# Optimization experiments

Measured on AMD Instinct MI355X. Metric: run time of the kernel, lower is better.

Reference implementation:

```python
import jax, jax.numpy as jnp
import numpy as np

LN_EPS = 1e-5

def sin_emb(coords, dim):
    # coords [..., 3] -> [..., dim]; dim split evenly over 3 axes, sin/cos halves
    per_axis = dim // 3
    half = per_axis // 2
    freqs = jnp.exp(-jnp.log(10000.0) * jnp.arange(half, dtype=coords.dtype) / max(half - 1, 1))
    ang = coords[..., None] * freqs  # [..., 3, half]
    emb = jnp.concatenate([jnp.sin(ang), jnp.cos(ang)], axis=-1)  # [..., 3, per_axis]
    return emb.reshape(coords.shape[:-1] + (dim,))

def layernorm(x, g, b):
    mu = jnp.mean(x, axis=-1, keepdims=True)
    var = jnp.mean((x - mu) ** 2, axis=-1, keepdims=True)
    return (x - mu) * jax.lax.rsqrt(var + LN_EPS) * g + b

def point_mlp(x, w, b, g, be, act):
    h = layernorm(x @ w + b, g, be)
    return jax.nn.gelu(h, approximate=False) if act else h

def query_ball_point(radius, nsample, xyz):
    # xyz [B,N,3] -> idx [B,N,nsample] (pad with first in-ball index, PointNet++ style)
    N = xyz.shape[1]
    sq = jnp.sum((xyz[:, :, None, :] - xyz[:, None, :, :]) ** 2, axis=-1)  # [B,N,N]
    idx0 = jnp.where(sq > radius * radius, N, jnp.arange(N)[None, None, :])
    idx = jnp.sort(idx0, axis=-1)[:, :, :nsample]
    return jnp.where(idx == N, idx[:, :, :1], idx)

def index_points(points, idx):
    # points [B,N,C], idx [B,S,K] -> [B,S,K,C]
    return jax.vmap(lambda p, i: p[i])(points, idx)

def setup_inputs() -> dict:
    key = jax.random.key(0)
    ks = jax.random.split(key, 20)
    B, N, C_stem, C_tok = 4, 4096, 64, 256
    C_in = C_stem + 3 + 24 + 96  # 187
    w = lambda k, i, o: jax.random.normal(k, (i, o), jnp.float32) * 0.02
    inp = {
        'xyz': jax.random.uniform(ks[0], (B, N, 3), jnp.float32),
        'point_feature': jax.random.normal(ks[1], (B, N, C_stem), jnp.float32),
        # scene_point_mlp
        'w1': w(ks[2], C_in, C_tok), 'b1': jnp.zeros((C_tok,)), 'g1': jnp.ones((C_tok,)), 'be1': jnp.zeros((C_tok,)),
        'w2': w(ks[3], C_tok, C_tok), 'b2': jnp.zeros((C_tok,)), 'g2': jnp.ones((C_tok,)), 'be2': jnp.zeros((C_tok,)),
        # scene_projection
        'pw1': w(ks[4], C_tok, C_tok), 'pb1': jnp.zeros((C_tok,)), 'pg1': jnp.ones((C_tok,)), 'pbe1': jnp.zeros((C_tok,)),
        'pw2': w(ks[5], C_tok, C_tok), 'pb2': jnp.zeros((C_tok,)), 'pg2': jnp.ones((C_tok,)), 'pbe2': jnp.zeros((C_tok,)),
    }
    return inp

def reference(xyz, point_feature, w1, b1, g1, be1, w2, b2, g2, be2,
              pw1, pb1, pg1, pbe1, pw2, pb2, pg2, pbe2):
    radius, K = 0.16, 32
    idx = query_ball_point(radius, K, xyz)                     # [B,N,K]
    grouped_xyz = index_points(xyz, idx)                       # [B,N,K,3]
    grouped_feature = index_points(point_feature, idx)         # [B,N,K,Cs]
    relative_xyz = grouped_xyz - xyz[:, :, None, :]            # [B,N,K,3]
    relative_position = sin_emb(relative_xyz, 24)              # [B,N,K,24]
    absolute_position = sin_emb(xyz, 96)                       # [B,N,96]
    B, N = xyz.shape[0], xyz.shape[1]
    absolute_position = jnp.broadcast_to(absolute_position[:, :, None, :], (B, N, K, 96))
    grouped_input = jnp.concatenate(
        (grouped_feature, relative_xyz, relative_position, absolute_position), axis=-1)
    h = point_mlp(grouped_input, w1, b1, g1, be1, True)
    h = point_mlp(h, w2, b2, g2, be2, False)
    scene_point_feature = jnp.max(h, axis=2)                   # [B,N,C]
    pooled = jnp.max(scene_point_feature, axis=1, keepdims=True)  # [B,1,C]
    t = point_mlp(pooled, pw1, pb1, pg1, pbe1, True)
    global_scene_token = point_mlp(t, pw2, pb2, pg2, pbe2, False)
    return global_scene_token
```

## Files before the change

### kernel.cpp

```cpp
#include <hip/hip_runtime.h>
#include <hip/hip_bf16.h>
#include <math.h>


#define LN_EPS 1e-5f

typedef __attribute__((ext_vector_type(8))) short bf16x8;
typedef __attribute__((ext_vector_type(4))) float f32x4;
typedef __attribute__((ext_vector_type(2))) unsigned int u32x2;
typedef __attribute__((ext_vector_type(4))) unsigned int u32x4;

#if __has_builtin(__builtin_amdgcn_rcpf)
#define FRCP(x) __builtin_amdgcn_rcpf(x)
#else
#define FRCP(x) (1.0f / (x))
#endif

__device__ __forceinline__ unsigned short f2bf(float f) {
    unsigned int x = __float_as_uint(f);
    return (unsigned short)((x + 0x7FFFu + ((x >> 16) & 1u)) >> 16);
}
__device__ __forceinline__ unsigned int pack2(float a, float b) {
    union { __hip_bfloat162 h; unsigned int u; } cvt;
    cvt.h = __float22bfloat162_rn(make_float2(a, b));
    return cvt.u;
}
__device__ __forceinline__ unsigned int fenc(float f) {
    unsigned int u = __float_as_uint(f);
    return (u & 0x80000000u) ? ~u : (u | 0x80000000u);
}
__device__ __forceinline__ float fdec(unsigned int u) {
    return __uint_as_float((u & 0x80000000u) ? (u & 0x7FFFFFFFu) : ~u);
}
__device__ __forceinline__ float gelu_fast(float x) {
    float x2 = x * x;
    float u = x * fmaf(0.0356774081f, x2, 0.7978845608f);
    float e = exp2f(u * -2.8853900818f);
    float r = FRCP(e + 1.0f);
    return x * r;
}
template<int CTRL>
__device__ __forceinline__ float dppadd(float s) {
    int v = __builtin_amdgcn_update_dpp(0, __float_as_int(s), CTRL, 0xF, 0xF, true);
    return s + __int_as_float(v);
}
__device__ __forceinline__ float rowsum16(float x) {
    x = dppadd<0x128>(x);
    x = dppadd<0x124>(x);
    x = dppadd<0x122>(x);
    x = dppadd<0x121>(x);
    return x;
}

__global__ __launch_bounds__(256) void k_prep(
    const float* __restrict__ w1, const float* __restrict__ w2,
    unsigned short* __restrict__ w2T, unsigned short* __restrict__ w1aT,
    unsigned short* __restrict__ w1cT, unsigned short* __restrict__ w1bT,
    unsigned int* __restrict__ pooled, int* __restrict__ done)
{
    int t = threadIdx.x, blk = blockIdx.x;
    if (blk < 16) {
        __shared__ unsigned short tile[64][65];
        int tr = blk >> 2, tc = blk & 3;
        #pragma unroll
        for (int rr = 0; rr < 16; ++rr) {
            int kl = rr * 4 + (t >> 6), nl = t & 63;
            tile[kl][nl] = f2bf(w2[(size_t)(tr * 64 + kl) * 256 + tc * 64 + nl]);
        }
        __syncthreads();
        #pragma unroll
        for (int rr = 0; rr < 16; ++rr) {
            int nl = rr * 4 + (t >> 6), kp = t & 63;
            int kl = (kp & 3) * 16 + (kp >> 2);
            w2T[(size_t)(tc * 64 + nl) * 256 + tr * 64 + kp] = tile[kl][nl];
        }
    } else if (blk < 20) {
        __shared__ unsigned short tile[64][65];
        int tc = blk - 16;
        #pragma unroll
        for (int rr = 0; rr < 16; ++rr) {
            int kl = rr * 4 + (t >> 6), nl = t & 63;
            tile[kl][nl] = f2bf(w1[(size_t)kl * 256 + tc * 64 + nl]);
        }
        __syncthreads();
        #pragma unroll
        for (int rr = 0; rr < 16; ++rr) {
            int nl = rr * 4 + (t >> 6), kl = t & 63;
            w1aT[(size_t)(tc * 64 + nl) * 64 + kl] = tile[kl][nl];
        }
    } else if (blk < 28) {
        __shared__ unsigned short tile[64][65];
        int idx = blk - 20;
        int tr2 = idx >> 2, tc = idx & 3;
        #pragma unroll
        for (int rr = 0; rr < 16; ++rr) {
            int kl = rr * 4 + (t >> 6), nl = t & 63;
            int k = tr2 * 64 + kl;
            float v = 0.f;
            if (k < 96) v = w1[(size_t)(91 + k) * 256 + tc * 64 + nl];
            tile[kl][nl] = f2bf(v);
        }
        __syncthreads();
        #pragma unroll
        for (int rr = 0; rr < 16; ++rr) {
            int nl = rr * 4 + (t >> 6), kl = t & 63;
            int k = tr2 * 64 + kl;
            if (k < 96)
                w1cT[(size_t)(tc * 64 + nl) * 96 + k] = tile[kl][nl];
        }
    } else if (blk == 28) {
        int n = t;
        #pragma unroll
        for (int k = 0; k < 32; ++k) {
            unsigned short v = 0;
            if (k < 27) v = f2bf(w1[(size_t)(64 + k) * 256 + n]);
            w1bT[(size_t)n * 32 + k] = v;
        }
    } else {
        unsigned int idv = fenc(-1e19f);
        for (int q = t; q < 1024; q += 256) pooled[q] = idv;
        if (t == 0) *done = 0;
    }
}

__global__ __launch_bounds__(256) void k_pre(
    const float* __restrict__ xyz, const float* __restrict__ pf,
    const unsigned short* __restrict__ w1aT, const unsigned short* __restrict__ w1cT,
    const float* __restrict__ b1,
    float* __restrict__ U_p, float* __restrict__ V_p)
{
    __shared__ __align__(16) unsigned short ptile[64 * 72];
    __shared__ __align__(16) unsigned short etile[64 * 104];
    int tid = threadIdx.x, wv = tid >> 6, lane = tid & 63;
    int lo16 = lane & 15, quad = lane >> 4;
    int rows0 = blockIdx.x * 64;

    {
        int r = tid >> 2, seg = tid & 3;
        const f32x4* src = (const f32x4*)(pf + (size_t)(rows0 + r) * 64 + seg * 16);
        f32x4 v0 = src[0], v1 = src[1], v2 = src[2], v3 = src[3];
        u32x4 o0, o1;
        o0.x = pack2(v0.x, v0.y); o0.y = pack2(v0.z, v0.w);
        o0.z = pack2(v1.x, v1.y); o0.w = pack2(v1.z, v1.w);
        o1.x = pack2(v2.x, v2.y); o1.y = pack2(v2.z, v2.w);
        o1.z = pack2(v3.x, v3.y); o1.w = pack2(v3.z, v3.w);
        u32x4* dst = (u32x4*)&ptile[r * 72 + seg * 16];
        dst[0] = o0; dst[1] = o1;
    }
    {
        int r = tid & 63, grp = tid >> 6;
        float c0 = xyz[(size_t)(rows0 + r) * 3];
        float c1 = xyz[(size_t)(rows0 + r) * 3 + 1];
        float c2 = xyz[(size_t)(rows0 + r) * 3 + 2];
        #pragma unroll
        for (int q = 0; q < 12; ++q) {
            int pr = grp * 12 + q;
            float vals[2];
            #pragma unroll
            for (int qq = 0; qq < 2; ++qq) {
                int cc = pr * 2 + qq;
                int a = cc >> 5, wI = cc & 31;
                int jf = (wI < 16) ? wI : (wI - 16);
                float coord = (a == 0) ? c0 : ((a == 1) ? c1 : c2);
                float fr = __expf(-0.61402269146507894f * (float)jf);
                float ang = coord * fr;
                vals[qq] = (wI < 16) ? __sinf(ang) : __cosf(ang);
            }
            *(unsigned int*)&etile[r * 104 + 2 * pr] = pack2(vals[0], vals[1]);
        }
    }
    __syncthreads();

    f32x4 acc[4][4];
    #pragma unroll
    for (int mt = 0; mt < 4; ++mt)
        #pragma unroll
        for (int nt = 0; nt < 4; ++nt) acc[mt][nt] = (f32x4){0.f, 0.f, 0.f, 0.f};
    #pragma unroll
    for (int ks = 0; ks < 2; ++ks) {
        bf16x8 bfr[4];
        #pragma unroll
        for (int nt = 0; nt < 4; ++nt) {
            int n = wv * 64 + nt * 16 + lo16;
            bfr[nt] = *(const bf16x8*)&w1aT[(size_t)n * 64 + ks * 32 + quad * 8];
        }
        #pragma unroll
        for (int mt = 0; mt < 4; ++mt) {
            bf16x8 afr = *(const bf16x8*)&ptile[(mt * 16 + lo16) * 72 + ks * 32 + quad * 8];
            #pragma unroll
            for (int nt = 0; nt < 4; ++nt)
                acc[mt][nt] = __builtin_amdgcn_mfma_f32_16x16x32_bf16(
                    afr, bfr[nt], acc[mt][nt], 0, 0, 0);
        }
    }
    #pragma unroll
    for (int mt = 0; mt < 4; ++mt)
        #pragma unroll
        for (int reg = 0; reg < 4; ++reg) {
            f32x4 o = {acc[mt][0][reg], acc[mt][1][reg], acc[mt][2][reg], acc[mt][3][reg]};
            *(f32x4*)&U_p[(size_t)(rows0 + mt * 16 + quad * 4 + reg) * 256 + wv * 64 + lo16 * 4] = o;
        }

    {
        float b1f[4];
        #pragma unroll
        for (int nt = 0; nt < 4; ++nt) b1f[nt] = b1[wv * 64 + nt * 16 + lo16];
        #pragma unroll
        for (int mt = 0; mt < 4; ++mt)
            #pragma unroll
            for (int nt = 0; nt < 4; ++nt)
                #pragma unroll
                for (int reg = 0; reg < 4; ++reg) acc[mt][nt][reg] = b1f[nt];
    }
    #pragma unroll
    for (int ks = 0; ks < 3; ++ks) {
        bf16x8 bfr[4];
        #pragma unroll
        for (int nt = 0; nt < 4; ++nt) {
            int n = wv * 64 + nt * 16 + lo16;
            bfr[nt] = *(const bf16x8*)&w1cT[(size_t)n * 96 + ks * 32 + quad * 8];
        }
        #pragma unroll
        for (int mt = 0; mt < 4; ++mt) {
            bf16x8 afr = *(const bf16x8*)&etile[(mt * 16 + lo16) * 104 + ks * 32 + quad * 8];
            #pragma unroll
            for (int nt = 0; nt < 4; ++nt)
                acc[mt][nt] = __builtin_amdgcn_mfma_f32_16x16x32_bf16(
                    afr, bfr[nt], acc[mt][nt], 0, 0, 0);
        }
    }
    #pragma unroll
    for (int mt = 0; mt < 4; ++mt)
        #pragma unroll
        for (int reg = 0; reg < 4; ++reg) {
            f32x4 o = {acc[mt][0][reg], acc[mt][1][reg], acc[mt][2][reg], acc[mt][3][reg]};
            *(f32x4*)&V_p[(size_t)(rows0 + mt * 16 + quad * 4 + reg) * 256 + wv * 64 + lo16 * 4] = o;
        }
}

__global__ __launch_bounds__(512, 4) void k_main(
    const float* __restrict__ xyz,
    const unsigned short* __restrict__ w1bT, const unsigned short* __restrict__ w2T,
    const float* __restrict__ U_p, const float* __restrict__ V_p,
    const float* __restrict__ g1, const float* __restrict__ be1,
    const float* __restrict__ b2, const float* __restrict__ g2,
    const float* __restrict__ be2,
    unsigned int* __restrict__ pooled, int* __restrict__ done,
    const float* __restrict__ pw1, const float* __restrict__ pb1,
    const float* __restrict__ pg1, const float* __restrict__ pbe1,
    const float* __restrict__ pw2, const float* __restrict__ pb2,
    const float* __restrict__ pg2, const float* __restrict__ pbe2,
    float* __restrict__ out)
{
    __shared__ __align__(16) unsigned short smem[128 * 264];
    __shared__ unsigned long long bmask[4][64];
    __shared__ int   idxs[128];
    __shared__ float ctr[4][3];
    __shared__ float reds[128][4][2];
    __shared__ float musig[128][2];
    __shared__ int   lastf;
    unsigned short* rels = smem;
    unsigned short* h1s  = smem;

    const int N = 4096;
    int tid = threadIdx.x, wv = tid >> 6, lane = tid & 63;
    int lo16 = lane & 15, quad = lane >> 4;
    int wvM = wv >> 2, wvN = wv & 3;
    int b = blockIdx.x & 3;
    int i0 = (blockIdx.x >> 2) * 4;
    size_t base = (size_t)b * N;
    const float* xb = xyz + base * 3;

    bf16x8 bfrR[4];
    #pragma unroll
    for (int nt = 0; nt < 4; ++nt) {
        int n = wvN * 64 + nt * 16 + lo16;
        bfrR[nt] = *(const bf16x8*)&w1bT[(size_t)n * 32 + quad * 8];
    }

    if (tid < 12) { int p = tid / 3, a = tid - 3 * p; ctr[p][a] = xb[(i0 + p) * 3 + a]; }
    const double r2d = 0.16 * 0.16;
    float T = (float)r2d;
    if ((double)T > r2d) T = __uint_as_float(__float_as_uint(T) - 1u);
    {
        f32x4 cA = *(const f32x4*)(xb + (size_t)i0 * 3);
        f32x4 cB = *(const f32x4*)(xb + (size_t)i0 * 3 + 4);
        f32x4 cC = *(const f32x4*)(xb + (size_t)i0 * 3 + 8);
        float cx0 = cA.x, cy0 = cA.y, cz0 = cA.z;
        float cx1 = cA.w, cy1 = cB.x, cz1 = cB.y;
        float cx2 = cB.z, cy2 = cB.w, cz2 = cC.x;
        float cx3 = cC.y, cy3 = cC.z, cz3 = cC.w;
        #pragma unroll 2
        for (int i = 0; i < 8; ++i) {
            int chunk = wv * 8 + i;
            int j = chunk * 64 + lane;
            const float* pp = xb + (size_t)j * 3;
            float px = pp[0], py = pp[1], pz = pp[2];
            float dx0 = __fsub_rn(px, cx0), dy0 = __fsub_rn(py, cy0), dz0 = __fsub_rn(pz, cz0);
            float sq0 = __fadd_rn(__fadd_rn(__fmul_rn(dx0, dx0), __fmul_rn(dy0, dy0)),
                                  __fmul_rn(dz0, dz0));
            unsigned long long m0 = __ballot(sq0 <= T);
            float dx1 = __fsub_rn(px, cx1), dy1 = __fsub_rn(py, cy1), dz1 = __fsub_rn(pz, cz1);
            float sq1 = __fadd_rn(__fadd_rn(__fmul_rn(dx1, dx1), __fmul_rn(dy1, dy1)),
                                  __fmul_rn(dz1, dz1));
            unsigned long long m1 = __ballot(sq1 <= T);
            float dx2 = __fsub_rn(px, cx2), dy2 = __fsub_rn(py, cy2), dz2 = __fsub_rn(pz, cz2);
            float sq2 = __fadd_rn(__fadd_rn(__fmul_rn(dx2, dx2), __fmul_rn(dy2, dy2)),
                                  __fmul_rn(dz2, dz2));
            unsigned long long m2 = __ballot(sq2 <= T);
            float dx3 = __fsub_rn(px, cx3), dy3 = __fsub_rn(py, cy3), dz3 = __fsub_rn(pz, cz3);
            float sq3 = __fadd_rn(__fadd_rn(__fmul_rn(dx3, dx3), __fmul_rn(dy3, dy3)),
                                  __fmul_rn(dz3, dz3));
            unsigned long long m3 = __ballot(sq3 <= T);
            if (lane == 0) {
                bmask[0][chunk] = m0; bmask[1][chunk] = m1;
                bmask[2][chunk] = m2; bmask[3][chunk] = m3;
            }
        }
    }
    __syncthreads();
    if (wv < 4) {
        int p = wv;
        unsigned long long m = bmask[p][lane];
        int c = __popcll(m);
        int inc = c;
        #pragma unroll
        for (int d = 1; d <= 32; d <<= 1) {
            int v = __shfl_up(inc, d);
            if (lane >= d) inc += v;
        }
        int exc = inc - c;
        int total = __shfl(inc, 63);
        unsigned long long lm = __ballot(m != 0ull);
        int fl = __ffsll(lm) - 1;
        unsigned long long mf = (unsigned long long)__shfl((long long)m, fl);
        int firstj = fl * 64 + __ffsll(mf) - 1;
        unsigned long long mm = m;
        int t = 0;
        while (mm != 0ull && (exc + t) < 32) {
            int bpos = __ffsll(mm) - 1;
            idxs[p * 32 + exc + t] = lane * 64 + bpos;
            mm &= mm - 1; ++t;
        }
        if (lane >= total && lane < 32) idxs[p * 32 + lane] = firstj;
    }
    __syncthreads();

    {
        int r = tid & 127, part = tid >> 7;
        int p = r >> 5;
        int j = idxs[r];
        float rx = xb[j * 3]     - ctr[p][0];
        float ry = xb[j * 3 + 1] - ctr[p][1];
        float rz = xb[j * 3 + 2] - ctr[p][2];
        unsigned short* arow = &rels[r * 40];
        if (part == 0) {
            *(unsigned int*)&arow[0] = pack2(rx, ry);
            arow[2] = f2bf(rz);
            arow[27] = 0;
            *(u32x2*)&arow[28] = (u32x2){0u, 0u};
        } else {
            int a = part - 1;
            float cv = (a == 0) ? rx : ((a == 1) ? ry : rz);
            const float fr4[4] = {1.f, 0.046415888336127774f,
                                  0.0021544346900318843f, 1e-4f};
            float sn[4], cs[4];
            #pragma unroll
            for (int tt = 0; tt < 4; ++tt) {
                float ang = cv * fr4[tt];
                sn[tt] = __sinf(ang); cs[tt] = __cosf(ang);
            }
            arow[3 + a * 8 + 0] = f2bf(sn[0]); arow[3 + a * 8 + 1] = f2bf(sn[1]);
            arow[3 + a * 8 + 2] = f2bf(sn[2]); arow[3 + a * 8 + 3] = f2bf(sn[3]);
            arow[3 + a * 8 + 4] = f2bf(cs[0]); arow[3 + a * 8 + 5] = f2bf(cs[1]);
            arow[3 + a * 8 + 6] = f2bf(cs[2]); arow[3 + a * 8 + 7] = f2bf(cs[3]);
        }
    }
    __syncthreads();

    const int arow0 = wvM * 64;
    f32x4 acc[4][4];
    #pragma unroll
    for (int mt = 0; mt < 4; ++mt) {
        int cl = wvM * 2 + (mt >> 1);
        f32x4 vv = *(const f32x4*)&V_p[(size_t)(base + i0 + cl) * 256 + wvN * 64 + lo16 * 4];
        #pragma unroll
        for (int reg = 0; reg < 4; ++reg) {
            int r = arow0 + mt * 16 + quad * 4 + reg;
            int j = idxs[r];
            f32x4 uu = *(const f32x4*)&U_p[(size_t)(base + j) * 256 + wvN * 64 + lo16 * 4];
            #pragma unroll
            for (int nt = 0; nt < 4; ++nt) acc[mt][nt][reg] = uu[nt] + vv[nt];
        }
    }
    #pragma unroll
    for (int mt = 0; mt < 4; ++mt) {
        bf16x8 afr = *(const bf16x8*)&rels[(arow0 + mt * 16 + lo16) * 40 + quad * 8];
        #pragma unroll
        for (int nt = 0; nt < 4; ++nt)
            acc[mt][nt] = __builtin_amdgcn_mfma_f32_16x16x32_bf16(
                afr, bfrR[nt], acc[mt][nt], 0, 0, 0);
    }

    #pragma unroll
    for (int mt = 0; mt < 4; ++mt) {
        #pragma unroll
        for (int reg = 0; reg < 4; ++reg) {
            float s1 = 0.f, s2 = 0.f;
            #pragma unroll
            for (int nt = 0; nt < 4; ++nt) { float v = acc[mt][nt][reg]; s1 += v; s2 = fmaf(v, v, s2); }
            s1 = rowsum16(s1); s2 = rowsum16(s2);
            if (lo16 == 0) {
                int r = arow0 + mt * 16 + quad * 4 + reg;
                reds[r][wvN][0] = s1; reds[r][wvN][1] = s2;
            }
        }
    }
    __syncthreads();
    if (tid < 128) {
        int r = tid;
        float s1 = reds[r][0][0] + reds[r][1][0] + reds[r][2][0] + reds[r][3][0];
        float s2 = reds[r][0][1] + reds[r][1][1] + reds[r][2][1] + reds[r][3][1];
        float mu = s1 * (1.f / 256.f);
        float var = fmaxf(s2 * (1.f / 256.f) - mu * mu, 0.f);
        musig[r][0] = mu; musig[r][1] = rsqrtf(var + LN_EPS);
    }
    __syncthreads();
    {
        float g1f[4], be1f[4];
        #pragma unroll
        for (int nt = 0; nt < 4; ++nt) {
            int n = wvN * 64 + nt * 16 + lo16;
            g1f[nt] = g1[n]; be1f[nt] = be1[n];
        }
        #pragma unroll
        for (int mt = 0; mt < 4; ++mt) {
            #pragma unroll
            for (int reg = 0; reg < 4; ++reg) {
                int r = arow0 + mt * 16 + quad * 4 + reg;
                float mu = musig[r][0], rs = musig[r][1];
                float v0 = gelu_fast(fmaf((acc[mt][0][reg] - mu) * rs, g1f[0], be1f[0]));
                float v1 = gelu_fast(fmaf((acc[mt][1][reg] - mu) * rs, g1f[1], be1f[1]));
                float v2 = gelu_fast(fmaf((acc[mt][2][reg] - mu) * rs, g1f[2], be1f[2]));
                float v3 = gelu_fast(fmaf((acc[mt][3][reg] - mu) * rs, g1f[3], be1f[3]));
                u32x2 w; w.x = pack2(v0, v1); w.y = pack2(v2, v3);
                *(u32x2*)&h1s[r * 264 + wvN * 64 + lo16 * 4] = w;
            }
        }
    }
    __syncthreads();

    {
        float b2f[4];
        #pragma unroll
        for (int nt = 0; nt < 4; ++nt) b2f[nt] = b2[wvN * 64 + nt * 16 + lo16];
        #pragma unroll
        for (int mt = 0; mt < 4; ++mt)
            #pragma unroll
            for (int nt = 0; nt < 4; ++nt)
                #pragma unroll
                for (int reg = 0; reg < 4; ++reg) acc[mt][nt][reg] = b2f[nt];
    }
    for (int ks = 0; ks < 8; ++ks) {
        bf16x8 bfr[4], afr[4];
        #pragma unroll
        for (int nt = 0; nt < 4; ++nt) {
            int n = wvN * 64 + nt * 16 + lo16;
            bfr[nt] = *(const bf16x8*)&w2T[(size_t)n * 256 + ks * 32 + quad * 8];
        }
        #pragma unroll
        for (int mt = 0; mt < 4; ++mt)
            afr[mt] = *(const bf16x8*)&h1s[(arow0 + mt * 16 + lo16) * 264 + ks * 32 + quad * 8];
        #pragma unroll
        for (int mt = 0; mt < 4; ++mt)
            #pragma unroll
            for (int nt = 0; nt < 4; ++nt)
                acc[mt][nt] = __builtin_amdgcn_mfma_f32_16x16x32_bf16(
                    afr[mt], bfr[nt], acc[mt][nt], 0, 0, 0);
    }

    {
        #pragma unroll
        for (int mt = 0; mt < 4; ++mt) {
            #pragma unroll
            for (int reg = 0; reg < 4; ++reg) {
                float s1 = 0.f, s2 = 0.f;
                #pragma unroll
                for (int nt = 0; nt < 4; ++nt) { float v = acc[mt][nt][reg]; s1 += v; s2 = fmaf(v, v, s2); }
                s1 = rowsum16(s1); s2 = rowsum16(s2);
                if (lo16 == 0) {
                    int r = arow0 + mt * 16 + quad * 4 + reg;
                    reds[r][wvN][0] = s1; reds[r][wvN][1] = s2;
                }
            }
        }
        __syncthreads();
        if (tid < 128) {
            int r = tid;
            float s1 = reds[r][0][0] + reds[r][1][0] + reds[r][2][0] + reds[r][3][0];
            float s2 = reds[r][0][1] + reds[r][1][1] + reds[r][2][1] + reds[r][3][1];
            float mu = s1 * (1.f / 256.f);
            float var = fmaxf(s2 * (1.f / 256.f) - mu * mu, 0.f);
            musig[r][0] = mu; musig[r][1] = rsqrtf(var + LN_EPS);
        }
        __syncthreads();

        float g2f[4], be2f[4];
        #pragma unroll
        for (int nt = 0; nt < 4; ++nt) {
            int n = wvN * 64 + nt * 16 + lo16;
            g2f[nt] = g2[n]; be2f[nt] = be2[n];
        }
        float mx[4] = {-1e30f, -1e30f, -1e30f, -1e30f};
        #pragma unroll
        for (int mt = 0; mt < 4; ++mt) {
            #pragma unroll
            for (int reg = 0; reg < 4; ++reg) {
                int r = arow0 + mt * 16 + quad * 4 + reg;
                float mu = musig[r][0], rs = musig[r][1];
                #pragma unroll
                for (int nt = 0; nt < 4; ++nt) {
                    float v = fmaf((acc[mt][nt][reg] - mu) * rs, g2f[nt], be2f[nt]);
                    mx[nt] = fmaxf(mx[nt], v);
                }
            }
        }
        #pragma unroll
        for (int nt = 0; nt < 4; ++nt) {
            mx[nt] = fmaxf(mx[nt], __shfl_xor(mx[nt], 16));
            mx[nt] = fmaxf(mx[nt], __shfl_xor(mx[nt], 32));
        }
        if (quad == 0) {
            #pragma unroll
            for (int nt = 0; nt < 4; ++nt)
                atomicMax(pooled + b * 256 + wvN * 64 + nt * 16 + lo16, fenc(mx[nt]));
        }
    }

    __syncthreads();
    if (tid == 0) lastf = (atomicAdd(done, 1) == 4095);
    __syncthreads();
    if (!lastf) return;
    if (wv < 4) {
        int bb = wv;
        float* xw = (float*)smem + wv * 512;
        #pragma unroll
        for (int q = 0; q < 4; ++q)
            xw[q * 64 + lane] =
                fdec(atomicMax(&pooled[bb * 256 + q * 64 + lane], 0u));

        float a1[4];
        #pragma unroll
        for (int q = 0; q < 4; ++q) a1[q] = pb1[q * 64 + lane];
        #pragma unroll 4
        for (int k = 0; k < 256; ++k) {
            float xv = xw[k];
            const float* wr = pw1 + (size_t)k * 256 + lane;
            #pragma unroll
            for (int q = 0; q < 4; ++q) a1[q] = fmaf(xv, wr[q * 64], a1[q]);
        }
        float s1 = a1[0] + a1[1] + a1[2] + a1[3];
        float s2 = fmaf(a1[0], a1[0], fmaf(a1[1], a1[1],
                   fmaf(a1[2], a1[2], a1[3] * a1[3])));
        s1 = rowsum16(s1); s2 = rowsum16(s2);
        s1 += __shfl_xor(s1, 16); s2 += __shfl_xor(s2, 16);
        s1 += __shfl_xor(s1, 32); s2 += __shfl_xor(s2, 32);
        float mu = s1 * (1.f / 256.f);
        float rs = rsqrtf(fmaxf(s2 * (1.f / 256.f) - mu * mu, 0.f) + LN_EPS);
        #pragma unroll
        for (int q = 0; q < 4; ++q) {
            int c = q * 64 + lane;
            xw[256 + c] = gelu_fast(fmaf((a1[q] - mu) * rs, pg1[c], pbe1[c]));
        }

        float a2[4];
        #pragma unroll
        for (int q = 0; q < 4; ++q) a2[q] = pb2[q * 64 + lane];
        #pragma unroll 4
        for (int k = 0; k < 256; ++k) {
            float xv = xw[256 + k];
            const float* wr = pw2 + (size_t)k * 256 + lane;
            #pragma unroll
            for (int q = 0; q < 4; ++q) a2[q] = fmaf(xv, wr[q * 64], a2[q]);
        }
        s1 = a2[0] + a2[1] + a2[2] + a2[3];
        s2 = fmaf(a2[0], a2[0], fmaf(a2[1], a2[1],
             fmaf(a2[2], a2[2], a2[3] * a2[3])));
        s1 = rowsum16(s1); s2 = rowsum16(s2);
        s1 += __shfl_xor(s1, 16); s2 += __shfl_xor(s2, 16);
        s1 += __shfl_xor(s1, 32); s2 += __shfl_xor(s2, 32);
        mu = s1 * (1.f / 256.f);
        rs = rsqrtf(fmaxf(s2 * (1.f / 256.f) - mu * mu, 0.f) + LN_EPS);
        #pragma unroll
        for (int q = 0; q < 4; ++q) {
            int c = q * 64 + lane;
            out[bb * 256 + c] = fmaf((a2[q] - mu) * rs, pg2[c], pbe2[c]);
        }
    }
}

extern "C" void kernel_launch(void* const* d_in, const int* in_sizes, int n_in,
                              void* d_out, int out_size, void* d_ws, size_t ws_size,
                              hipStream_t stream)
{
    char* ws = (char*)d_ws;
    unsigned short* w2T    = (unsigned short*)ws;
    unsigned short* w1aT   = (unsigned short*)(ws + (128u << 10));
    unsigned short* w1cT   = (unsigned short*)(ws + (160u << 10));
    unsigned short* w1bT   = (unsigned short*)(ws + (208u << 10));
    unsigned int*   pooled = (unsigned int*)(ws + (224u << 10));
    int*            done   = (int*)(ws + (228u << 10));
    float*          U_p    = (float*)(ws + (256u << 10));
    float*          V_p    = (float*)(ws + (256u << 10) + (16u << 20));

    const float* xyz = (const float*)d_in[0];
    const float* pf  = (const float*)d_in[1];
    const float* w1  = (const float*)d_in[2];
    const float* b1  = (const float*)d_in[3];

    k_prep<<<30, 256, 0, stream>>>(w1, (const float*)d_in[6],
                                   w2T, w1aT, w1cT, w1bT, pooled, done);
    k_pre<<<256, 256, 0, stream>>>(xyz, pf, w1aT, w1cT, b1, U_p, V_p);
    k_main<<<4096, 512, 0, stream>>>(xyz, w1bT, w2T, U_p, V_p,
                                     (const float*)d_in[4], (const float*)d_in[5],
                                     (const float*)d_in[7], (const float*)d_in[8],
                                     (const float*)d_in[9], pooled, done,
                                     (const float*)d_in[10], (const float*)d_in[11],
                                     (const float*)d_in[12], (const float*)d_in[13],
                                     (const float*)d_in[14], (const float*)d_in[15],
                                     (const float*)d_in[16], (const float*)d_in[17],
                                     (float*)d_out);
}
```

Measured before the change: 407.2 us.

## Reduce pooled max in shared memory, replicate global atomics, move final MLP to kernel

Each block now first reduces its per-wave maxima into a shared-memory pool, then issues one global atomicMax per channel into one of eight replicated pooled buffers. This cuts contention on the 1024 global pooled slots. The done-counter and last-block detection are replaced by a separate single-block k_final kernel that merges the eight replicas and runs the projection MLP. This adds one kernel launch and an extra block-wide sync plus shared-memory atomics per block.

```diff
diff --git a/kernel.cpp b/kernel.cpp
--- a/kernel.cpp
+++ b/kernel.cpp
@@ -56,7 +56,7 @@
     const float* __restrict__ w1, const float* __restrict__ w2,
     unsigned short* __restrict__ w2T, unsigned short* __restrict__ w1aT,
     unsigned short* __restrict__ w1cT, unsigned short* __restrict__ w1bT,
-    unsigned int* __restrict__ pooled, int* __restrict__ done)
+    unsigned int* __restrict__ pooled_r)
 {
     int t = threadIdx.x, blk = blockIdx.x;
     if (blk < 16) {
@@ -118,8 +118,7 @@
         }
     } else {
         unsigned int idv = fenc(-1e19f);
-        for (int q = t; q < 1024; q += 256) pooled[q] = idv;
-        if (t == 0) *done = 0;
+        for (int q = t; q < 8192; q += 256) pooled_r[q] = idv;
     }
 }
 
@@ -245,12 +244,7 @@
     const float* __restrict__ g1, const float* __restrict__ be1,
     const float* __restrict__ b2, const float* __restrict__ g2,
     const float* __restrict__ be2,
-    unsigned int* __restrict__ pooled, int* __restrict__ done,
-    const float* __restrict__ pw1, const float* __restrict__ pb1,
-    const float* __restrict__ pg1, const float* __restrict__ pbe1,
-    const float* __restrict__ pw2, const float* __restrict__ pb2,
-    const float* __restrict__ pg2, const float* __restrict__ pbe2,
-    float* __restrict__ out)
+    unsigned int* __restrict__ pooled_r)
 {
     __shared__ __align__(16) unsigned short smem[128 * 264];
     __shared__ unsigned long long bmask[4][64];
@@ -258,7 +252,7 @@
     __shared__ float ctr[4][3];
     __shared__ float reds[128][4][2];
     __shared__ float musig[128][2];
-    __shared__ int   lastf;
+    __shared__ unsigned int pool_s[256];
     unsigned short* rels = smem;
     unsigned short* h1s  = smem;
 
@@ -268,6 +262,7 @@
     int wvM = wv >> 2, wvN = wv & 3;
     int b = blockIdx.x & 3;
     int i0 = (blockIdx.x >> 2) * 4;
+    int rep = (blockIdx.x >> 2) & 7;
     size_t base = (size_t)b * N;
     const float* xb = xyz + base * 3;
 
@@ -278,6 +273,7 @@
         bfrR[nt] = *(const bf16x8*)&w1bT[(size_t)n * 32 + quad * 8];
     }
 
+    if (tid < 256) pool_s[tid] = fenc(-1e19f);
     if (tid < 12) { int p = tid / 3, a = tid - 3 * p; ctr[p][a] = xb[(i0 + p) * 3 + a]; }
     const double r2d = 0.16 * 0.16;
     float T = (float)r2d;
@@ -533,69 +529,85 @@
         if (quad == 0) {
             #pragma unroll
             for (int nt = 0; nt < 4; ++nt)
-                atomicMax(pooled + b * 256 + wvN * 64 + nt * 16 + lo16, fenc(mx[nt]));
-        }
-    }
-
-    __syncthreads();
-    if (tid == 0) lastf = (atomicAdd(done, 1) == 4095);
-    __syncthreads();
-    if (!lastf) return;
-    if (wv < 4) {
-        int bb = wv;
-        float* xw = (float*)smem + wv * 512;
-        #pragma unroll
-        for (int q = 0; q < 4; ++q)
-            xw[q * 64 + lane] =
-                fdec(atomicMax(&pooled[bb * 256 + q * 64 + lane], 0u));
-
-        float a1[4];
-        #pragma unroll
-        for (int q = 0; q < 4; ++q) a1[q] = pb1[q * 64 + lane];
-        #pragma unroll 4
-        for (int k = 0; k < 256; ++k) {
-            float xv = xw[k];
-            const float* wr = pw1 + (size_t)k * 256 + lane;
-            #pragma unroll
-            for (int q = 0; q < 4; ++q) a1[q] = fmaf(xv, wr[q * 64], a1[q]);
-        }
-        float s1 = a1[0] + a1[1] + a1[2] + a1[3];
-        float s2 = fmaf(a1[0], a1[0], fmaf(a1[1], a1[1],
-                   fmaf(a1[2], a1[2], a1[3] * a1[3])));
-        s1 = rowsum16(s1); s2 = rowsum16(s2);
-        s1 += __shfl_xor(s1, 16); s2 += __shfl_xor(s2, 16);
-        s1 += __shfl_xor(s1, 32); s2 += __shfl_xor(s2, 32);
-        float mu = s1 * (1.f / 256.f);
-        float rs = rsqrtf(fmaxf(s2 * (1.f / 256.f) - mu * mu, 0.f) + LN_EPS);
-        #pragma unroll
-        for (int q = 0; q < 4; ++q) {
-            int c = q * 64 + lane;
-            xw[256 + c] = gelu_fast(fmaf((a1[q] - mu) * rs, pg1[c], pbe1[c]));
-        }
-
-        float a2[4];
-        #pragma unroll
-        for (int q = 0; q < 4; ++q) a2[q] = pb2[q * 64 + lane];
-        #pragma unroll 4
-        for (int k = 0; k < 256; ++k) {
-            float xv = xw[256 + k];
-            const float* wr = pw2 + (size_t)k * 256 + lane;
-            #pragma unroll
-            for (int q = 0; q < 4; ++q) a2[q] = fmaf(xv, wr[q * 64], a2[q]);
-        }
-        s1 = a2[0] + a2[1] + a2[2] + a2[3];
-        s2 = fmaf(a2[0], a2[0], fmaf(a2[1], a2[1],
-             fmaf(a2[2], a2[2], a2[3] * a2[3])));
-        s1 = rowsum16(s1); s2 = rowsum16(s2);
-        s1 += __shfl_xor(s1, 16); s2 += __shfl_xor(s2, 16);
-        s1 += __shfl_xor(s1, 32); s2 += __shfl_xor(s2, 32);
-        mu = s1 * (1.f / 256.f);
-        rs = rsqrtf(fmaxf(s2 * (1.f / 256.f) - mu * mu, 0.f) + LN_EPS);
-        #pragma unroll
-        for (int q = 0; q < 4; ++q) {
-            int c = q * 64 + lane;
-            out[bb * 256 + c] = fmaf((a2[q] - mu) * rs, pg2[c], pbe2[c]);
-        }
+                atomicMax(&pool_s[wvN * 64 + nt * 16 + lo16], fenc(mx[nt]));
+        }
+    }
+    __syncthreads();
+    if (tid < 256)
+        atomicMax(pooled_r + rep * 1024 + b * 256 + tid, pool_s[tid]);
+}
+
+__global__ __launch_bounds__(256) void k_final(
+    const unsigned int* __restrict__ pooled_r,
+    const float* __restrict__ pw1, const float* __restrict__ pb1,
+    const float* __restrict__ pg1, const float* __restrict__ pbe1,
+    const float* __restrict__ pw2, const float* __restrict__ pb2,
+    const float* __restrict__ pg2, const float* __restrict__ pbe2,
+    float* __restrict__ out)
+{
+    __shared__ float xw4[4][512];
+    int tid = threadIdx.x, wv = tid >> 6, lane = tid & 63;
+    int bb = wv;
+    float* xw = xw4[wv];
+
+    #pragma unroll
+    for (int q = 0; q < 4; ++q) {
+        int c = q * 64 + lane;
+        unsigned int mv = pooled_r[bb * 256 + c];
+        #pragma unroll
+        for (int r = 1; r < 8; ++r) {
+            unsigned int v = pooled_r[r * 1024 + bb * 256 + c];
+            mv = (v > mv) ? v : mv;
+        }
+        xw[c] = fdec(mv);
+    }
+
+    float a1[4];
+    #pragma unroll
+    for (int q = 0; q < 4; ++q) a1[q] = pb1[q * 64 + lane];
+    #pragma unroll 4
+    for (int k = 0; k < 256; ++k) {
+        float xv = xw[k];
+        const float* wr = pw1 + (size_t)k * 256 + lane;
+        #pragma unroll
+        for (int q = 0; q < 4; ++q) a1[q] = fmaf(xv, wr[q * 64], a1[q]);
+    }
+    float s1 = a1[0] + a1[1] + a1[2] + a1[3];
+    float s2 = fmaf(a1[0], a1[0], fmaf(a1[1], a1[1],
+               fmaf(a1[2], a1[2], a1[3] * a1[3])));
+    s1 = rowsum16(s1); s2 = rowsum16(s2);
+    s1 += __shfl_xor(s1, 16); s2 += __shfl_xor(s2, 16);
+    s1 += __shfl_xor(s1, 32); s2 += __shfl_xor(s2, 32);
+    float mu = s1 * (1.f / 256.f);
+    float rs = rsqrtf(fmaxf(s2 * (1.f / 256.f) - mu * mu, 0.f) + LN_EPS);
+    #pragma unroll
+    for (int q = 0; q < 4; ++q) {
+        int c = q * 64 + lane;
+        xw[256 + c] = gelu_fast(fmaf((a1[q] - mu) * rs, pg1[c], pbe1[c]));
+    }
+
+    float a2[4];
+    #pragma unroll
+    for (int q = 0; q < 4; ++q) a2[q] = pb2[q * 64 + lane];
+    #pragma unroll 4
+    for (int k = 0; k < 256; ++k) {
+        float xv = xw[256 + k];
+        const float* wr = pw2 + (size_t)k * 256 + lane;
+        #pragma unroll
+        for (int q = 0; q < 4; ++q) a2[q] = fmaf(xv, wr[q * 64], a2[q]);
+    }
+    s1 = a2[0] + a2[1] + a2[2] + a2[3];
+    s2 = fmaf(a2[0], a2[0], fmaf(a2[1], a2[1],
+         fmaf(a2[2], a2[2], a2[3] * a2[3])));
+    s1 = rowsum16(s1); s2 = rowsum16(s2);
+    s1 += __shfl_xor(s1, 16); s2 += __shfl_xor(s2, 16);
+    s1 += __shfl_xor(s1, 32); s2 += __shfl_xor(s2, 32);
+    mu = s1 * (1.f / 256.f);
+    rs = rsqrtf(fmaxf(s2 * (1.f / 256.f) - mu * mu, 0.f) + LN_EPS);
+    #pragma unroll
+    for (int q = 0; q < 4; ++q) {
+        int c = q * 64 + lane;
+        out[bb * 256 + c] = fmaf((a2[q] - mu) * rs, pg2[c], pbe2[c]);
     }
 }
 
@@ -604,14 +616,13 @@
                               hipStream_t stream)
 {
     char* ws = (char*)d_ws;
-    unsigned short* w2T    = (unsigned short*)ws;
-    unsigned short* w1aT   = (unsigned short*)(ws + (128u << 10));
-    unsigned short* w1cT   = (unsigned short*)(ws + (160u << 10));
-    unsigned short* w1bT   = (unsigned short*)(ws + (208u << 10));
-    unsigned int*   pooled = (unsigned int*)(ws + (224u << 10));
-    int*            done   = (int*)(ws + (228u << 10));
-    float*          U_p    = (float*)(ws + (256u << 10));
-    float*          V_p    = (float*)(ws + (256u << 10) + (16u << 20));
+    unsigned short* w2T      = (unsigned short*)ws;
+    unsigned short* w1aT     = (unsigned short*)(ws + (128u << 10));
+    unsigned short* w1cT     = (unsigned short*)(ws + (160u << 10));
+    unsigned short* w1bT     = (unsigned short*)(ws + (208u << 10));
+    unsigned int*   pooled_r = (unsigned int*)(ws + (224u << 10));
+    float*          U_p      = (float*)(ws + (256u << 10));
+    float*          V_p      = (float*)(ws + (256u << 10) + (16u << 20));
 
     const float* xyz = (const float*)d_in[0];
     const float* pf  = (const float*)d_in[1];
@@ -619,15 +630,16 @@
     const float* b1  = (const float*)d_in[3];
 
     k_prep<<<30, 256, 0, stream>>>(w1, (const float*)d_in[6],
-                                   w2T, w1aT, w1cT, w1bT, pooled, done);
+                                   w2T, w1aT, w1cT, w1bT, pooled_r);
     k_pre<<<256, 256, 0, stream>>>(xyz, pf, w1aT, w1cT, b1, U_p, V_p);
     k_main<<<4096, 512, 0, stream>>>(xyz, w1bT, w2T, U_p, V_p,
                                      (const float*)d_in[4], (const float*)d_in[5],
                                      (const float*)d_in[7], (const float*)d_in[8],
-                                     (const float*)d_in[9], pooled, done,
-                                     (const float*)d_in[10], (const float*)d_in[11],
-                                     (const float*)d_in[12], (const float*)d_in[13],
-                                     (const float*)d_in[14], (const float*)d_in[15],
-                                     (const float*)d_in[16], (const float*)d_in[17],
-                                     (float*)d_out);
-}
+                                     (const float*)d_in[9], pooled_r);
+    k_final<<<1, 256, 0, stream>>>(pooled_r,
+                                   (const float*)d_in[10], (const float*)d_in[11],
+                                   (const float*)d_in[12], (const float*)d_in[13],
+                                   (const float*)d_in[14], (const float*)d_in[15],
+                                   (const float*)d_in[16], (const float*)d_in[17],
+                                   (float*)d_out);
+}
```

Result: no change. 402.0 us (-1.3%).
